# Optimization experiments

Hardware: AMD Instinct MI355X
Metric: run time of the kernel (lower is better)

## Reference

```python
import jax, jax.numpy as jnp
import numpy as np

SCENE = (256, 256, 32)     # scene_size from SLCF-Net docstring (256*256*32 voxels)
PROJECT_SCALE = 1
C, H, W = 64, 480, 640
N = SCENE[0] * SCENE[1] * SCENE[2]


def setup_inputs() -> dict:
    key = jax.random.key(0)
    k1, k2, k3, k4, k5 = jax.random.split(key, 5)
    x2d = jax.random.normal(k1, (C, H, W), dtype=jnp.float32)
    # pix coords in [0, 480) -> valid for both x (<640) and y (<480)
    projected_pix = jax.random.randint(k2, (N, 2), 0, 480, dtype=jnp.int32)
    fov_mask = jax.random.bernoulli(k3, 0.7, (N,))
    pix_z = jax.random.uniform(k4, (N,), dtype=jnp.float32) * 50.0
    depth_img = jax.random.uniform(k5, (1, H, W), dtype=jnp.float32) * 50.0
    return {
        "x2d": x2d,
        "projected_pix": projected_pix,
        "scale_2d": 1,
        "fov_mask": fov_mask,
        "pix_z": pix_z,
        "depth_img": depth_img,
    }


def reference(x2d, projected_pix, scale_2d, fov_mask, pix_z, depth_img):
    c, h, w = x2d.shape
    pix_x = projected_pix[:, 0]
    pix_y = projected_pix[:, 1]

    # --- feature gather (out-of-FOV voxels map to the appended zero column) ---
    sx = pix_x // scale_2d
    sy = pix_y // scale_2d
    feat_idx = sy * w + sx                                  # (N,)
    src = x2d.reshape(c, -1)                                # (c, h*w)
    src_feature = jnp.where(fov_mask[None, :], src[:, feat_idx], jnp.float32(0.0))  # (c, N)

    # --- depth gather (out-of-FOV voxels map to the appended zero entry) ---
    dep_idx = pix_y * w + pix_x                             # (N,)
    depth_flat = depth_img.reshape(-1)                      # (h*w,)
    depth_values = jnp.where(fov_mask, depth_flat[dep_idx], jnp.float32(0.0))       # (N,)

    # --- gaussian decay weight, mu=0, sigma=1/project_scale; depth==0 -> weight 1 ---
    sigma = jnp.float32(1.0 / PROJECT_SCALE)
    gw = jnp.exp(jnp.float32(-0.5) * ((pix_z - depth_values) / sigma) ** 2)
    weights = jnp.where(depth_values == 0.0, jnp.float32(1.0), gw)                  # (N,)

    weighted = src_feature * weights[None, :]               # (c, N)
    s = PROJECT_SCALE
    return weighted.reshape(c, SCENE[0] // s, SCENE[1] // s, SCENE[2] // s)
```

## Files before the change

kernel.cpp:

```cpp
#include <hip/hip_runtime.h>

#define NVOX (256*256*32)
#define CC 64
#define HH 480
#define WW 640
#define HWTOT (HH*WW)

typedef float vfloat4 __attribute__((ext_vector_type(4)));
typedef int   vint4   __attribute__((ext_vector_type(4)));
typedef int   vint2   __attribute__((ext_vector_type(2)));
typedef _Float16 f16x4 __attribute__((ext_vector_type(4)));
typedef _Float16 f16x8 __attribute__((ext_vector_type(8)));

__global__ __launch_bounds__(256) void transpose_f16_kernel(
    const float* __restrict__ x2d,
    _Float16*    __restrict__ xT)
{
    __shared__ float tile[64][65];
    int t  = threadIdx.x;
    int p0 = blockIdx.x * 64;

#pragma unroll
    for (int k = 0; k < 4; ++k) {
        int idx = k * 256 + t;
        int c   = idx >> 4;
        int pg  = idx & 15;
        vfloat4 v = __builtin_nontemporal_load(
            (const vfloat4*)(x2d + (long)c * HWTOT + p0) + pg);
        tile[c][pg*4+0] = v.x;
        tile[c][pg*4+1] = v.y;
        tile[c][pg*4+2] = v.z;
        tile[c][pg*4+3] = v.w;
    }
    __syncthreads();
#pragma unroll
    for (int k = 0; k < 4; ++k) {
        int idx = k * 256 + t;
        int p   = idx >> 4;
        int cg  = idx & 15;
        f16x4 h;
        h[0] = (_Float16)tile[cg*4+0][p];
        h[1] = (_Float16)tile[cg*4+1][p];
        h[2] = (_Float16)tile[cg*4+2][p];
        h[3] = (_Float16)tile[cg*4+3][p];
        ((f16x4*)(xT + (long)(p0 + p) * CC))[cg] = h;
    }
}

__device__ __forceinline__ void emit8(float* op, f16x8 v, float w, int c0) {
#pragma unroll
    for (int j = 0; j < 8; ++j) {
        float f = (float)v[j] * w;
        __builtin_nontemporal_store(f, op + (long)(c0 + j) * NVOX);
    }
}

__global__ __launch_bounds__(256) void gather_f16_kernel(
    const _Float16* __restrict__ xT,
    const int*      __restrict__ pp,
    const int*      __restrict__ scale_p,
    const int*      __restrict__ mask,
    const float*    __restrict__ pix_z,
    const float*    __restrict__ depth,
    float*          __restrict__ out)
{
    int i = blockIdx.x * blockDim.x + threadIdx.x;
    int scale = scale_p[0];

    vint2 p2 = __builtin_nontemporal_load((const vint2*)pp + i);
    int   m  = __builtin_nontemporal_load(mask + i);
    float z  = __builtin_nontemporal_load(pix_z + i);

    int px = p2.x, py = p2.y;
    int sx = px, sy = py;
    if (scale != 1) { sx = px / scale; sy = py / scale; }
    bool fov = (m != 0);
    int  fi  = fov ? (sy * WW + sx) : 0;
    float d  = fov ? depth[py * WW + px] : 0.0f;
    float diff = z - d;
    float gw = __expf(-0.5f * diff * diff);
    float w  = (d == 0.0f) ? 1.0f : gw;
    w = fov ? w : 0.0f;

    const f16x8* src = (const f16x8*)(xT + (long)fi * CC);
    float* op = out + i;

    f16x8 s0 = src[0], s1 = src[1], s2 = src[2], s3 = src[3];
    f16x8 s4 = src[4], s5 = src[5], s6 = src[6], s7 = src[7];

    emit8(op, s0,  w,  0);
    emit8(op, s1,  w,  8);
    emit8(op, s2,  w, 16);
    emit8(op, s3,  w, 24);
    emit8(op, s4,  w, 32);
    emit8(op, s5,  w, 40);
    emit8(op, s6,  w, 48);
    emit8(op, s7,  w, 56);
}

__global__ __launch_bounds__(256) void fused_kernel(
    const float* __restrict__ x2d,
    const int*   __restrict__ pp,
    const int*   __restrict__ scale_p,
    const int*   __restrict__ mask,
    const float* __restrict__ pix_z,
    const float* __restrict__ depth,
    float*       __restrict__ out)
{
    int t = blockIdx.x * blockDim.x + threadIdx.x;
    long i0 = (long)t * 4;
    int cg = blockIdx.y * 4;
    int scale = scale_p[0];

    vint4 pp0 = ((const vint4*)pp)[t*2+0];
    vint4 pp1 = ((const vint4*)pp)[t*2+1];
    vint4 m4  = ((const vint4*)mask)[t];
    vfloat4 z4 = ((const vfloat4*)pix_z)[t];

    int   px[4] = {pp0.x, pp0.z, pp1.x, pp1.z};
    int   py[4] = {pp0.y, pp0.w, pp1.y, pp1.w};
    int   mm[4] = {m4.x, m4.y, m4.z, m4.w};
    float zz[4] = {z4.x, z4.y, z4.z, z4.w};

    int fi[4]; float wv[4];
#pragma unroll
    for (int j = 0; j < 4; ++j) {
        int sx = px[j], sy = py[j];
        if (scale != 1) { sx = px[j] / scale; sy = py[j] / scale; }
        int feat = sy * WW + sx;
        bool fov = (mm[j] != 0);
        float d = fov ? depth[py[j] * WW + px[j]] : 0.0f;
        float diff = zz[j] - d;
        float gw = __expf(-0.5f * diff * diff);
        float w = (d == 0.0f) ? 1.0f : gw;
        wv[j] = fov ? w : 0.0f;
        fi[j] = fov ? feat : 0;
    }

#pragma unroll
    for (int g = 0; g < 4; ++g) {
        int c = cg + g;
        const float* base = x2d + (long)c * HWTOT;
        vfloat4 v;
        v.x = base[fi[0]] * wv[0];
        v.y = base[fi[1]] * wv[1];
        v.z = base[fi[2]] * wv[2];
        v.w = base[fi[3]] * wv[3];
        __builtin_nontemporal_store(v, (vfloat4*)(out + (long)c * NVOX + i0));
    }
}

extern "C" void kernel_launch(void* const* d_in, const int* in_sizes, int n_in,
                              void* d_out, int out_size, void* d_ws, size_t ws_size,
                              hipStream_t stream) {
    const float* x2d     = (const float*)d_in[0];
    const int*   pp      = (const int*)d_in[1];
    const int*   scale_p = (const int*)d_in[2];
    const int*   mask    = (const int*)d_in[3];
    const float* pix_z   = (const float*)d_in[4];
    const float* depth   = (const float*)d_in[5];
    float*       out     = (float*)d_out;

    dim3 blk(256);
    size_t need_xT = (size_t)HWTOT * CC * sizeof(_Float16);

    if (ws_size >= need_xT) {
        _Float16* xT = (_Float16*)d_ws;
        transpose_f16_kernel<<<dim3(HWTOT/64), blk, 0, stream>>>(x2d, xT);
        gather_f16_kernel<<<dim3(NVOX/256), blk, 0, stream>>>(xT, pp, scale_p,
                                                              mask, pix_z, depth, out);
    } else {
        fused_kernel<<<dim3(NVOX/4/256, CC/4), blk, 0, stream>>>(x2d, pp, scale_p,
                                                                 mask, pix_z, depth, out);
    }
}
```

Before: 673.1 us.

## Split gather into channel slices with precomputed index/weight metadata

```diff
diff --git a/kernel.cpp b/kernel.cpp
--- a/kernel.cpp
+++ b/kernel.cpp
@@ -6,63 +6,22 @@
 #define WW 640
 #define HWTOT (HH*WW)
 
+#define SLICES 8
+#define CPS 8
+
 typedef float vfloat4 __attribute__((ext_vector_type(4)));
 typedef int   vint4   __attribute__((ext_vector_type(4)));
 typedef int   vint2   __attribute__((ext_vector_type(2)));
 typedef _Float16 f16x4 __attribute__((ext_vector_type(4)));
 typedef _Float16 f16x8 __attribute__((ext_vector_type(8)));
 
-__global__ __launch_bounds__(256) void transpose_f16_kernel(
-    const float* __restrict__ x2d,
-    _Float16*    __restrict__ xT)
-{
-    __shared__ float tile[64][65];
-    int t  = threadIdx.x;
-    int p0 = blockIdx.x * 64;
-
-#pragma unroll
-    for (int k = 0; k < 4; ++k) {
-        int idx = k * 256 + t;
-        int c   = idx >> 4;
-        int pg  = idx & 15;
-        vfloat4 v = __builtin_nontemporal_load(
-            (const vfloat4*)(x2d + (long)c * HWTOT + p0) + pg);
-        tile[c][pg*4+0] = v.x;
-        tile[c][pg*4+1] = v.y;
-        tile[c][pg*4+2] = v.z;
-        tile[c][pg*4+3] = v.w;
-    }
-    __syncthreads();
-#pragma unroll
-    for (int k = 0; k < 4; ++k) {
-        int idx = k * 256 + t;
-        int p   = idx >> 4;
-        int cg  = idx & 15;
-        f16x4 h;
-        h[0] = (_Float16)tile[cg*4+0][p];
-        h[1] = (_Float16)tile[cg*4+1][p];
-        h[2] = (_Float16)tile[cg*4+2][p];
-        h[3] = (_Float16)tile[cg*4+3][p];
-        ((f16x4*)(xT + (long)(p0 + p) * CC))[cg] = h;
-    }
-}
-
-__device__ __forceinline__ void emit8(float* op, f16x8 v, float w, int c0) {
-#pragma unroll
-    for (int j = 0; j < 8; ++j) {
-        float f = (float)v[j] * w;
-        __builtin_nontemporal_store(f, op + (long)(c0 + j) * NVOX);
-    }
-}
-
-__global__ __launch_bounds__(256) void gather_f16_kernel(
-    const _Float16* __restrict__ xT,
-    const int*      __restrict__ pp,
-    const int*      __restrict__ scale_p,
-    const int*      __restrict__ mask,
-    const float*    __restrict__ pix_z,
-    const float*    __restrict__ depth,
-    float*          __restrict__ out)
+__global__ __launch_bounds__(256) void weight_kernel(
+    const int*   __restrict__ pp,
+    const int*   __restrict__ scale_p,
+    const int*   __restrict__ mask,
+    const float* __restrict__ pix_z,
+    const float* __restrict__ depth,
+    vint2*       __restrict__ meta)
 {
     int i = blockIdx.x * blockDim.x + threadIdx.x;
     int scale = scale_p[0];
@@ -82,30 +41,123 @@
     float w  = (d == 0.0f) ? 1.0f : gw;
     w = fov ? w : 0.0f;
 
+    vint2 o; o.x = fi; o.y = __float_as_int(w);
+    __builtin_nontemporal_store(o, meta + i);
+}
+
+__global__ __launch_bounds__(256) void transpose_slice_kernel(
+    const float* __restrict__ x2d,
+    _Float16*    __restrict__ xTs)
+{
+    __shared__ float tile[64][65];
+    int t  = threadIdx.x;
+    int p0 = blockIdx.x * 64;
+
+#pragma unroll
+    for (int k = 0; k < 4; ++k) {
+        int idx = k * 256 + t;
+        int c   = idx >> 4;
+        int pg  = idx & 15;
+        vfloat4 v = __builtin_nontemporal_load(
+            (const vfloat4*)(x2d + (long)c * HWTOT + p0) + pg);
+        tile[c][pg*4+0] = v.x;
+        tile[c][pg*4+1] = v.y;
+        tile[c][pg*4+2] = v.z;
+        tile[c][pg*4+3] = v.w;
+    }
+    __syncthreads();
+#pragma unroll
+    for (int k = 0; k < 4; ++k) {
+        int idx = k * 256 + t;
+        int p   = idx >> 4;
+        int cg  = idx & 15;
+        f16x4 h;
+        h[0] = (_Float16)tile[cg*4+0][p];
+        h[1] = (_Float16)tile[cg*4+1][p];
+        h[2] = (_Float16)tile[cg*4+2][p];
+        h[3] = (_Float16)tile[cg*4+3][p];
+        int s  = cg >> 1;
+        int j0 = (cg & 1) * 4;
+        *(f16x4*)(xTs + ((long)s * HWTOT + (p0 + p)) * CPS + j0) = h;
+    }
+}
+
+__global__ __launch_bounds__(256) void gather_slice_kernel(
+    const _Float16* __restrict__ xTs,
+    const vint2*    __restrict__ meta,
+    float*          __restrict__ out)
+{
+    int i = blockIdx.x * blockDim.x + threadIdx.x;
+    int s = blockIdx.y;
+
+    vint2 mw = __builtin_nontemporal_load(meta + i);
+    int   fi = mw.x;
+    float w  = __int_as_float(mw.y);
+
+    f16x8 v = *(const f16x8*)(xTs + ((long)s * HWTOT + fi) * CPS);
+    float* op = out + (long)s * CPS * NVOX + i;
+
+#pragma unroll
+    for (int j = 0; j < CPS; ++j) {
+        float f = (float)v[j] * w;
+        __builtin_nontemporal_store(f, op + (long)j * NVOX);
+    }
+}
+
+__global__ __launch_bounds__(256) void transpose_f16_kernel(
+    const float* __restrict__ x2d, _Float16* __restrict__ xT)
+{
+    __shared__ float tile[64][65];
+    int t  = threadIdx.x;
+    int p0 = blockIdx.x * 64;
+#pragma unroll
+    for (int k = 0; k < 4; ++k) {
+        int idx = k * 256 + t;
+        int c = idx >> 4, pg = idx & 15;
+        vfloat4 v = __builtin_nontemporal_load(
+            (const vfloat4*)(x2d + (long)c * HWTOT + p0) + pg);
+        tile[c][pg*4+0] = v.x; tile[c][pg*4+1] = v.y;
+        tile[c][pg*4+2] = v.z; tile[c][pg*4+3] = v.w;
+    }
+    __syncthreads();
+#pragma unroll
+    for (int k = 0; k < 4; ++k) {
+        int idx = k * 256 + t;
+        int p = idx >> 4, cg = idx & 15;
+        f16x4 h;
+        h[0] = (_Float16)tile[cg*4+0][p];
+        h[1] = (_Float16)tile[cg*4+1][p];
+        h[2] = (_Float16)tile[cg*4+2][p];
+        h[3] = (_Float16)tile[cg*4+3][p];
+        ((f16x4*)(xT + (long)(p0 + p) * CC))[cg] = h;
+    }
+}
+
+__global__ __launch_bounds__(256) void gather_f16_kernel(
+    const _Float16* __restrict__ xT, const vint2* __restrict__ meta,
+    float* __restrict__ out)
+{
+    int i = blockIdx.x * blockDim.x + threadIdx.x;
+    vint2 mw = __builtin_nontemporal_load(meta + i);
+    int fi = mw.x; float w = __int_as_float(mw.y);
     const f16x8* src = (const f16x8*)(xT + (long)fi * CC);
     float* op = out + i;
-
     f16x8 s0 = src[0], s1 = src[1], s2 = src[2], s3 = src[3];
     f16x8 s4 = src[4], s5 = src[5], s6 = src[6], s7 = src[7];
-
-    emit8(op, s0,  w,  0);
-    emit8(op, s1,  w,  8);
-    emit8(op, s2,  w, 16);
-    emit8(op, s3,  w, 24);
-    emit8(op, s4,  w, 32);
-    emit8(op, s5,  w, 40);
-    emit8(op, s6,  w, 48);
-    emit8(op, s7,  w, 56);
+    f16x8 ss[8] = {s0,s1,s2,s3,s4,s5,s6,s7};
+#pragma unroll
+    for (int g = 0; g < 8; ++g)
+#pragma unroll
+        for (int j = 0; j < 8; ++j)
+            __builtin_nontemporal_store((float)ss[g][j] * w,
+                                        op + (long)(8*g + j) * NVOX);
 }
 
 __global__ __launch_bounds__(256) void fused_kernel(
-    const float* __restrict__ x2d,
-    const int*   __restrict__ pp,
-    const int*   __restrict__ scale_p,
-    const int*   __restrict__ mask,
-    const float* __restrict__ pix_z,
-    const float* __restrict__ depth,
-    float*       __restrict__ out)
+    const float* __restrict__ x2d, const int* __restrict__ pp,
+    const int* __restrict__ scale_p, const int* __restrict__ mask,
+    const float* __restrict__ pix_z, const float* __restrict__ depth,
+    float* __restrict__ out)
 {
     int t = blockIdx.x * blockDim.x + threadIdx.x;
     long i0 = (long)t * 4;
@@ -162,13 +214,24 @@
     float*       out     = (float*)d_out;
 
     dim3 blk(256);
-    size_t need_xT = (size_t)HWTOT * CC * sizeof(_Float16);
-
-    if (ws_size >= need_xT) {
-        _Float16* xT = (_Float16*)d_ws;
+    size_t meta_bytes = (size_t)NVOX * 8;
+    size_t xT_bytes   = (size_t)HWTOT * CC * sizeof(_Float16);
+    size_t need_full  = meta_bytes + xT_bytes;
+
+    if (ws_size >= need_full) {
+        vint2*    meta = (vint2*)d_ws;
+        _Float16* xTs  = (_Float16*)((char*)d_ws + meta_bytes);
+        weight_kernel<<<dim3(NVOX/256), blk, 0, stream>>>(pp, scale_p, mask,
+                                                          pix_z, depth, meta);
+        transpose_slice_kernel<<<dim3(HWTOT/64), blk, 0, stream>>>(x2d, xTs);
+        gather_slice_kernel<<<dim3(NVOX/256, SLICES), blk, 0, stream>>>(xTs, meta, out);
+    } else if (ws_size >= xT_bytes + meta_bytes) {
+        vint2*    meta = (vint2*)d_ws;
+        _Float16* xT   = (_Float16*)((char*)d_ws + meta_bytes);
+        weight_kernel<<<dim3(NVOX/256), blk, 0, stream>>>(pp, scale_p, mask,
+                                                          pix_z, depth, meta);
         transpose_f16_kernel<<<dim3(HWTOT/64), blk, 0, stream>>>(x2d, xT);
-        gather_f16_kernel<<<dim3(NVOX/256), blk, 0, stream>>>(xT, pp, scale_p,
-                                                              mask, pix_z, depth, out);
+        gather_f16_kernel<<<dim3(NVOX/256), blk, 0, stream>>>(xT, meta, out);
     } else {
         fused_kernel<<<dim3(NVOX/4/256, CC/4), blk, 0, stream>>>(x2d, pp, scale_p,
                                                                  mask, pix_z, depth, out);
```

After: 693.1 us. +3.0%, slower.
